# Performance work log

Measured on AMD Instinct MI355X. Metric: run time of the kernel, lower is better.

Reference implementation:

```python
import jax, jax.numpy as jnp
import numpy as np
import math

D_MODEL, D_K, D_V, N_HEADS = 1024, 64, 64, 16
B, LQ, LK = 4, 2048, 2048
LN_EPS = 1e-5


def setup_inputs() -> dict:
    key = jax.random.key(0)
    ks = jax.random.split(key, 8)
    s = 1.0 / math.sqrt(D_MODEL)
    return {
        "input_Q": jax.random.normal(ks[0], (B, LQ, D_MODEL), jnp.float32),
        "input_K": jax.random.normal(ks[1], (B, LK, D_MODEL), jnp.float32),
        "input_V": jax.random.normal(ks[2], (B, LK, D_MODEL), jnp.float32),
        "attn_mask": jax.random.randint(ks[3], (B, LQ, LK), 0, 2).astype(bool),
        # weights stored as [in, out] (torch Linear applies x @ W.T)
        "W_Q": jax.random.normal(ks[4], (D_MODEL, N_HEADS * D_K), jnp.float32) * s,
        "W_K": jax.random.normal(ks[5], (D_MODEL, N_HEADS * D_K), jnp.float32) * s,
        "W_V": jax.random.normal(ks[6], (D_MODEL, N_HEADS * D_V), jnp.float32) * s,
        "W_fc": jax.random.normal(ks[7], (N_HEADS * D_V, D_MODEL), jnp.float32) * s,
    }


def reference(input_Q, input_K, input_V, attn_mask, W_Q, W_K, W_V, W_fc):
    b, lq, _ = input_Q.shape
    lk = input_K.shape[1]
    # projections -> [b, len, h, d] -> [b, h, len, d]
    Q = (input_Q @ W_Q).reshape(b, lq, N_HEADS, D_K).transpose(0, 2, 1, 3)
    K = (input_K @ W_K).reshape(b, lk, N_HEADS, D_K).transpose(0, 2, 1, 3)
    V = (input_V @ W_V).reshape(b, lk, N_HEADS, D_V).transpose(0, 2, 1, 3)
    # scaled scores [b, h, q, k]
    scores = jnp.einsum("bhqd,bhkd->bhqk", Q, K) / math.sqrt(D_K)
    scores = jnp.where(attn_mask[:, None, :, :], -1e9, scores)
    attn = jax.nn.softmax(scores, axis=-1)
    # context [b, h, q, dv] -> [b, q, h*dv]
    ctx = jnp.einsum("bhqk,bhkd->bhqd", attn, V)
    ctx = ctx.transpose(0, 2, 1, 3).reshape(b, lq, N_HEADS * D_V)
    result = ctx @ W_fc
    x = result + input_Q
    mu = jnp.mean(x, axis=-1, keepdims=True)
    var = jnp.var(x, axis=-1, keepdims=True)
    res = (x - mu) / jnp.sqrt(var + LN_EPS)
    return res, attn
```

## Files before the change

### kernel.cpp

```cpp
#include <hip/hip_runtime.h>
#include <hip/hip_bf16.h>
#include <stdint.h>

#define DEVI __device__ __forceinline__

typedef __attribute__((ext_vector_type(8))) short bf16x8;
typedef __attribute__((ext_vector_type(4))) float f32x4;

static DEVI unsigned short f2bf(float f) {
  unsigned int u = __builtin_bit_cast(unsigned int, f);
  u = (u + 0x7FFFu + ((u >> 16) & 1u)) >> 16;
  return (unsigned short)u;
}

static DEVI void async16(const void* g, void* l) {
  __builtin_amdgcn_global_load_lds((__attribute__((address_space(1))) void*)(g),
                                   (__attribute__((address_space(3))) void*)(l),
                                   16, 0, 0);
}

__global__ __launch_bounds__(256) void cvt_kernel(const float* __restrict__ in,
                                                  unsigned short* __restrict__ out, int n4) {
  int i = blockIdx.x * 256 + threadIdx.x;
  if (i >= n4) return;
  float4 v = ((const float4*)in)[i];
  uint2 o;
  o.x = (unsigned)f2bf(v.x) | ((unsigned)f2bf(v.y) << 16);
  o.y = (unsigned)f2bf(v.z) | ((unsigned)f2bf(v.w) << 16);
  ((uint2*)out)[i] = o;
}

__global__ __launch_bounds__(256) void maskbits_kernel(const int* __restrict__ mask,
                                                       unsigned long long* __restrict__ mb) {
  size_t tg = (size_t)blockIdx.x * 256 + threadIdx.x;
  int v = mask[tg];
  unsigned long long bal = __ballot(v != 0);
  if ((threadIdx.x & 63) == 0) mb[tg >> 6] = bal;
}

__global__ __launch_bounds__(256) void wtrans_kernel(const float* __restrict__ W,
                                                     unsigned short* __restrict__ Wt) {
  __shared__ float t[32][33];
  const int bx = blockIdx.x * 32;
  const int by = blockIdx.y * 32;
  const int tx = threadIdx.x, ty = threadIdx.y;
#pragma unroll
  for (int i = 0; i < 32; i += 8) t[ty + i][tx] = W[(size_t)(by + ty + i) * 1024 + bx + tx];
  __syncthreads();
#pragma unroll
  for (int i = 0; i < 32; i += 8)
    Wt[(size_t)(bx + ty + i) * 1024 + by + tx] = f2bf(t[tx][ty + i]);
}

template <bool OUT_F32>
__global__ __launch_bounds__(256) void gemm_nt(const unsigned short* __restrict__ A, int lda,
                                               const unsigned short* __restrict__ B, int ldb,
                                               void* __restrict__ Cp, int ldc, int K) {
  __shared__ unsigned short As[128 * 64];
  __shared__ unsigned short Bs[128 * 64];
  const int tid = threadIdx.x;
  const int wave = tid >> 6, lane = tid & 63;
  const int m0 = blockIdx.x * 128, n0 = blockIdx.y * 128;
  const int wr = (wave >> 1) * 64, wc = (wave & 1) * 64;
  const int fr = lane & 15, fg = lane >> 4;
  f32x4 acc[4][4] = {};
  for (int kt = 0; kt < K; kt += 64) {
    __syncthreads();
#pragma unroll
    for (int it = 0; it < 4; ++it) {
      int id = it * 256 + tid;
      int row = id >> 3, ch = id & 7;
      async16(A + (size_t)(m0 + row) * lda + kt + ch * 8,
              (char*)As + (it * 256 + wave * 64) * 16);
      async16(B + (size_t)(n0 + row) * ldb + kt + ch * 8,
              (char*)Bs + (it * 256 + wave * 64) * 16);
    }
    __syncthreads();
#pragma unroll
    for (int ks = 0; ks < 2; ++ks) {
      bf16x8 af[4], bfr[4];
#pragma unroll
      for (int i = 0; i < 4; ++i)
        af[i] = *(const bf16x8*)(As + (wr + i * 16 + fr) * 64 + ks * 32 + fg * 8);
#pragma unroll
      for (int j = 0; j < 4; ++j)
        bfr[j] = *(const bf16x8*)(Bs + (wc + j * 16 + fr) * 64 + ks * 32 + fg * 8);
#pragma unroll
      for (int i = 0; i < 4; ++i)
#pragma unroll
        for (int j = 0; j < 4; ++j)
          acc[i][j] = __builtin_amdgcn_mfma_f32_16x16x32_bf16(af[i], bfr[j], acc[i][j], 0, 0, 0);
    }
  }
#pragma unroll
  for (int i = 0; i < 4; ++i)
#pragma unroll
    for (int j = 0; j < 4; ++j)
#pragma unroll
      for (int r = 0; r < 4; ++r) {
        int row = m0 + wr + i * 16 + fg * 4 + r;
        int col = n0 + wc + j * 16 + fr;
        if (OUT_F32)
          ((float*)Cp)[(size_t)row * ldc + col] = acc[i][j][r];
        else
          ((unsigned short*)Cp)[(size_t)row * ldc + col] = f2bf(acc[i][j][r]);
      }
}

__global__ __launch_bounds__(256) void vtrans_kernel(const unsigned short* __restrict__ Vp,
                                                     unsigned short* __restrict__ Vt) {
  __shared__ unsigned short t[64][72];
  const int bh = blockIdx.y;
  const int b = bh >> 4, h = bh & 15;
  const int l0 = blockIdx.x * 64;
  const int tid = threadIdx.x;
#pragma unroll
  for (int it = 0; it < 2; ++it) {
    int id = it * 256 + tid;
    int l = id >> 3, ch = id & 7;
    uint4 v = *(const uint4*)(Vp + (size_t)(b * 2048 + l0 + l) * 1024 + h * 64 + ch * 8);
    *(uint4*)(&t[l][ch * 8]) = v;
  }
  __syncthreads();
#pragma unroll
  for (int it = 0; it < 2; ++it) {
    int id = it * 256 + tid;
    int d = id >> 3, lc = id & 7;
    unsigned short o[8];
#pragma unroll
    for (int k = 0; k < 8; ++k) o[k] = t[lc * 8 + k][d];
    uint4 ov;
    ov.x = o[0] | ((unsigned)o[1] << 16);
    ov.y = o[2] | ((unsigned)o[3] << 16);
    ov.z = o[4] | ((unsigned)o[5] << 16);
    ov.w = o[6] | ((unsigned)o[7] << 16);
    *(uint4*)(Vt + ((size_t)bh * 64 + d) * 2048 + l0 + lc * 8) = ov;
  }
}

__global__ __launch_bounds__(256) void attn_kernel(
    const unsigned short* __restrict__ Qp, const unsigned short* __restrict__ Kp,
    const unsigned short* __restrict__ Vt, const unsigned long long* __restrict__ mb,
    float* __restrict__ attn_out, unsigned short* __restrict__ ctx) {
  __shared__ unsigned short Ks[2][4096];
  __shared__ unsigned short Vs[2][4096];
  __shared__ unsigned short Ps[4][1024];
  const int tid = threadIdx.x, wave = tid >> 6, lane = tid & 63;
  const int g = blockIdx.x;
  const int idx = g >> 3;
  const int bh = (g & 7) * 8 + (idx >> 5);
  const int b = bh >> 4, h = bh & 15;
  const int q0 = (idx & 31) * 64;
  const int fr = lane & 15, fg = lane >> 4;
  const int q = q0 + wave * 16 + fr;

  const int r0 = tid >> 3;
  const int chs = ((tid & 7) ^ (r0 & 7)) << 3;
  const unsigned short* kg = Kp + (size_t)(b * 2048 + r0) * 1024 + h * 64 + chs;
  const unsigned short* vg = Vt + (size_t)bh * 131072 + (size_t)r0 * 2048 + chs;

#define STAGE_K(buf, t)                                                    \
  do {                                                                     \
    const unsigned short* _k = kg + (size_t)(t) * 65536;                   \
    async16(_k, (char*)Ks[buf] + wave * 1024);                             \
    async16(_k + 32768, (char*)Ks[buf] + 4096 + wave * 1024);              \
  } while (0)
#define STAGE_V(buf, t)                                                    \
  do {                                                                     \
    const unsigned short* _v = vg + (t) * 64;                              \
    async16(_v, (char*)Vs[buf] + wave * 1024);                             \
    async16(_v + 65536, (char*)Vs[buf] + 4096 + wave * 1024);              \
  } while (0)

  const int c0 = (fg ^ (fr & 7)) << 3;
  const int c1 = ((4 + fg) ^ (fr & 7)) << 3;
  const int psw = (fr & 7) << 3;

  const unsigned short* qbase = Qp + (size_t)(b * 2048 + q) * 1024 + h * 64 + fg * 8;
  bf16x8 qa0 = *(const bf16x8*)(qbase);
  bf16x8 qa1 = *(const bf16x8*)(qbase + 32);

  const unsigned long long* mrow = mb + (size_t)(b * 2048 + q) * 32;
  const int msh = fg * 4;

  STAGE_K(0, 0);
  int cur = 0;
  float rsum = 0.f;
  for (int kt = 0; kt < 32; ++kt) {
    unsigned long long mw = mrow[kt];
    STAGE_K(cur ^ 1, (kt + 1) & 31);
    asm volatile("s_waitcnt vmcnt(3)" ::: "memory");
    __builtin_amdgcn_s_barrier();
    f32x4 s[4] = {};
#pragma unroll
    for (int j = 0; j < 4; ++j) {
      bf16x8 k0 = *(const bf16x8*)(&Ks[cur][(j * 16 + fr) * 64 + c0]);
      bf16x8 k1 = *(const bf16x8*)(&Ks[cur][(j * 16 + fr) * 64 + c1]);
      s[j] = __builtin_amdgcn_mfma_f32_16x16x32_bf16(k0, qa0, s[j], 0, 0, 0);
      s[j] = __builtin_amdgcn_mfma_f32_16x16x32_bf16(k1, qa1, s[j], 0, 0, 0);
    }
    unsigned mlo = (unsigned)mw, mhi = (unsigned)(mw >> 32);
#pragma unroll
    for (int j = 0; j < 4; ++j) {
      unsigned mj = ((j & 2) ? mhi : mlo) >> ((j & 1) * 16 + msh);
      rsum += ((mj & 1) ? 0.f : exp2f(s[j][0] * 0.18033688f));
      rsum += ((mj & 2) ? 0.f : exp2f(s[j][1] * 0.18033688f));
      rsum += ((mj & 4) ? 0.f : exp2f(s[j][2] * 0.18033688f));
      rsum += ((mj & 8) ? 0.f : exp2f(s[j][3] * 0.18033688f));
    }
    asm volatile("s_waitcnt lgkmcnt(0)" ::: "memory");
    __builtin_amdgcn_s_barrier();
    cur ^= 1;
  }
  rsum += __shfl_xor(rsum, 16);
  rsum += __shfl_xor(rsum, 32);
  const float rs = 1.0f / rsum;

  STAGE_V(cur, 0);
  asm volatile("s_waitcnt vmcnt(0)" ::: "memory");
  __builtin_amdgcn_s_barrier();
  f32x4 o[4] = {};
  unsigned short* pw = Ps[wave];
  float* aout = attn_out + ((size_t)(bh * 2048 + q)) * 2048 + fg * 4;

  for (int kt = 0; kt < 32; ++kt) {
    unsigned long long mw = mrow[kt];
    STAGE_K(cur ^ 1, (kt + 1) & 31);
    STAGE_V(cur ^ 1, (kt + 1) & 31);
    asm volatile("s_waitcnt vmcnt(21)" ::: "memory");
    __builtin_amdgcn_s_barrier();
    f32x4 s[4] = {};
#pragma unroll
    for (int j = 0; j < 4; ++j) {
      bf16x8 k0 = *(const bf16x8*)(&Ks[cur][(j * 16 + fr) * 64 + c0]);
      bf16x8 k1 = *(const bf16x8*)(&Ks[cur][(j * 16 + fr) * 64 + c1]);
      s[j] = __builtin_amdgcn_mfma_f32_16x16x32_bf16(k0, qa0, s[j], 0, 0, 0);
      s[j] = __builtin_amdgcn_mfma_f32_16x16x32_bf16(k1, qa1, s[j], 0, 0, 0);
    }
    unsigned mlo = (unsigned)mw, mhi = (unsigned)(mw >> 32);
#pragma unroll
    for (int j = 0; j < 4; ++j) {
      unsigned mj = ((j & 2) ? mhi : mlo) >> ((j & 1) * 16 + msh);
      float e0 = (mj & 1) ? 0.f : exp2f(s[j][0] * 0.18033688f) * rs;
      float e1 = (mj & 2) ? 0.f : exp2f(s[j][1] * 0.18033688f) * rs;
      float e2 = (mj & 4) ? 0.f : exp2f(s[j][2] * 0.18033688f) * rs;
      float e3 = (mj & 8) ? 0.f : exp2f(s[j][3] * 0.18033688f) * rs;
      f32x4 ev;
      ev[0] = e0; ev[1] = e1; ev[2] = e2; ev[3] = e3;
      __builtin_nontemporal_store(ev, (f32x4*)(aout + kt * 64 + j * 16));
      uint2 pv;
      pv.x = (unsigned)f2bf(e0) | ((unsigned)f2bf(e1) << 16);
      pv.y = (unsigned)f2bf(e2) | ((unsigned)f2bf(e3) << 16);
      *(uint2*)(pw + fr * 64 + ((j * 16 + fg * 4) ^ psw)) = pv;
    }
    asm volatile("s_waitcnt lgkmcnt(0)" ::: "memory");
    __builtin_amdgcn_sched_barrier(0);
    bf16x8 pa0 = *(const bf16x8*)(pw + fr * 64 + ((fg * 8) ^ psw));
    bf16x8 pa1 = *(const bf16x8*)(pw + fr * 64 + ((32 + fg * 8) ^ psw));
#pragma unroll
    for (int ct = 0; ct < 4; ++ct) {
      bf16x8 v0 = *(const bf16x8*)(&Vs[cur][(ct * 16 + fr) * 64 + c0]);
      bf16x8 v1 = *(const bf16x8*)(&Vs[cur][(ct * 16 + fr) * 64 + c1]);
      o[ct] = __builtin_amdgcn_mfma_f32_16x16x32_bf16(pa0, v0, o[ct], 0, 0, 0);
      o[ct] = __builtin_amdgcn_mfma_f32_16x16x32_bf16(pa1, v1, o[ct], 0, 0, 0);
    }
    asm volatile("s_waitcnt lgkmcnt(0)" ::: "memory");
    __builtin_amdgcn_s_barrier();
    cur ^= 1;
  }
#pragma unroll
  for (int ct = 0; ct < 4; ++ct)
#pragma unroll
    for (int r = 0; r < 4; ++r)
      ctx[(size_t)(b * 2048 + q0 + wave * 16 + fg * 4 + r) * 1024 + h * 64 + ct * 16 + fr] =
          f2bf(o[ct][r]);
#undef STAGE_K
#undef STAGE_V
}

__global__ __launch_bounds__(256) void ln_kernel(const float* __restrict__ resl,
                                                 const float* __restrict__ inQ,
                                                 float* __restrict__ out) {
  __shared__ float red[8];
  const int row = blockIdx.x, tid = threadIdx.x;
  const int wave = tid >> 6, lane = tid & 63;
  float4 xv = ((const float4*)(resl + (size_t)row * 1024))[tid];
  float4 qv = ((const float4*)(inQ + (size_t)row * 1024))[tid];
  float v0 = xv.x + qv.x, v1 = xv.y + qv.y, v2 = xv.z + qv.z, v3 = xv.w + qv.w;
  float s = v0 + v1 + v2 + v3;
  float s2 = v0 * v0 + v1 * v1 + v2 * v2 + v3 * v3;
#pragma unroll
  for (int off = 1; off < 64; off <<= 1) {
    s += __shfl_xor(s, off);
    s2 += __shfl_xor(s2, off);
  }
  if (lane == 0) { red[wave] = s; red[4 + wave] = s2; }
  __syncthreads();
  s = red[0] + red[1] + red[2] + red[3];
  s2 = red[4] + red[5] + red[6] + red[7];
  const float mu = s * (1.0f / 1024.0f);
  const float var = s2 * (1.0f / 1024.0f) - mu * mu;
  const float inv = rsqrtf(var + 1e-5f);
  float4 ov;
  ov.x = (v0 - mu) * inv;
  ov.y = (v1 - mu) * inv;
  ov.z = (v2 - mu) * inv;
  ov.w = (v3 - mu) * inv;
  ((float4*)(out + (size_t)row * 1024))[tid] = ov;
}

extern "C" void kernel_launch(void* const* d_in, const int* in_sizes, int n_in, void* d_out,
                              int out_size, void* d_ws, size_t ws_size, hipStream_t stream) {
  const float* inQ = (const float*)d_in[0];
  const float* inK = (const float*)d_in[1];
  const float* inV = (const float*)d_in[2];
  const int* mask = (const int*)d_in[3];
  const float* WQ = (const float*)d_in[4];
  const float* WK = (const float*)d_in[5];
  const float* WV = (const float*)d_in[6];
  const float* WF = (const float*)d_in[7];
  float* res = (float*)d_out;
  float* attn = res + (size_t)8192 * 1024;

  char* w = (char*)d_ws;
  unsigned short* inQb = (unsigned short*)w; w += (size_t)16777216;
  unsigned short* inKb = (unsigned short*)w; w += (size_t)16777216;
  unsigned short* inVb = (unsigned short*)w; w += (size_t)16777216;
  unsigned short* WQt = (unsigned short*)w; w += (size_t)2097152;
  unsigned short* WKt = (unsigned short*)w; w += (size_t)2097152;
  unsigned short* WVt = (unsigned short*)w; w += (size_t)2097152;
  unsigned short* WFt = (unsigned short*)w; w += (size_t)2097152;
  unsigned short* Qp  = (unsigned short*)w; w += (size_t)16777216;
  unsigned short* Kp  = (unsigned short*)w; w += (size_t)16777216;
  unsigned short* Vp  = (unsigned short*)w; w += (size_t)16777216;
  unsigned short* Vtb = (unsigned short*)w; w += (size_t)16777216;
  unsigned short* ctx = (unsigned short*)w; w += (size_t)16777216;
  float* resl = (float*)w; w += (size_t)33554432;
  unsigned long long* mbits = (unsigned long long*)inQb;

  cvt_kernel<<<8192, 256, 0, stream>>>(inQ, inQb, 2097152);
  cvt_kernel<<<8192, 256, 0, stream>>>(inK, inKb, 2097152);
  cvt_kernel<<<8192, 256, 0, stream>>>(inV, inVb, 2097152);
  dim3 wb(32, 8);
  wtrans_kernel<<<dim3(32, 32), wb, 0, stream>>>(WQ, WQt);
  wtrans_kernel<<<dim3(32, 32), wb, 0, stream>>>(WK, WKt);
  wtrans_kernel<<<dim3(32, 32), wb, 0, stream>>>(WV, WVt);
  wtrans_kernel<<<dim3(32, 32), wb, 0, stream>>>(WF, WFt);
  gemm_nt<false><<<dim3(64, 8), 256, 0, stream>>>(inQb, 1024, WQt, 1024, Qp, 1024, 1024);
  gemm_nt<false><<<dim3(64, 8), 256, 0, stream>>>(inKb, 1024, WKt, 1024, Kp, 1024, 1024);
  gemm_nt<false><<<dim3(64, 8), 256, 0, stream>>>(inVb, 1024, WVt, 1024, Vp, 1024, 1024);
  maskbits_kernel<<<65536, 256, 0, stream>>>(mask, mbits);
  vtrans_kernel<<<dim3(32, 64), 256, 0, stream>>>(Vp, Vtb);
  attn_kernel<<<2048, 256, 0, stream>>>(Qp, Kp, Vtb, mbits, attn, ctx);
  gemm_nt<true><<<dim3(64, 8), 256, 0, stream>>>(ctx, 1024, WFt, 1024, resl, 1024, 1024);
  ln_kernel<<<8192, 256, 0, stream>>>(resl, inQ, res);
}
```

Baseline: 535.2 us.

## Process two query tiles per wave in attention to halve K/V staging

Each wave now handles 32 query rows (two 16-row groups) instead of 16, so each workgroup covers 128 queries and the grid is halved, reusing each staged K/V tile across twice the queries. The softmax scale (log2e/sqrt(dk)) is folded into W_Q during weight transposition, which removes a multiply per score. Masked entries become exp2(-inf) rather than a select after exp. The bf16 packing now uses a v_cvt_pk_bf16_f32 instruction. Register pressure rises with doubled accumulators, though launch bounds hint at 4 blocks per SIMD.

Result: slower. 588.4 us (+9.9%).

```diff
diff --git a/kernel.cpp b/kernel.cpp
--- a/kernel.cpp
+++ b/kernel.cpp
@@ -39,7 +39,8 @@
 }
 
 __global__ __launch_bounds__(256) void wtrans_kernel(const float* __restrict__ W,
-                                                     unsigned short* __restrict__ Wt) {
+                                                     unsigned short* __restrict__ Wt,
+                                                     float scale) {
   __shared__ float t[32][33];
   const int bx = blockIdx.x * 32;
   const int by = blockIdx.y * 32;
@@ -49,7 +50,7 @@
   __syncthreads();
 #pragma unroll
   for (int i = 0; i < 32; i += 8)
-    Wt[(size_t)(bx + ty + i) * 1024 + by + tx] = f2bf(t[tx][ty + i]);
+    Wt[(size_t)(bx + ty + i) * 1024 + by + tx] = f2bf(t[tx][ty + i] * scale);
 }
 
 template <bool OUT_F32>
@@ -138,7 +139,7 @@
   }
 }
 
-__global__ __launch_bounds__(256) void attn_kernel(
+__global__ __launch_bounds__(256, 4) void attn_kernel(
     const unsigned short* __restrict__ Qp, const unsigned short* __restrict__ Kp,
     const unsigned short* __restrict__ Vt, const unsigned long long* __restrict__ mb,
     float* __restrict__ attn_out, unsigned short* __restrict__ ctx) {
@@ -148,11 +149,12 @@
   const int tid = threadIdx.x, wave = tid >> 6, lane = tid & 63;
   const int g = blockIdx.x;
   const int idx = g >> 3;
-  const int bh = (g & 7) * 8 + (idx >> 5);
+  const int bh = (g & 7) * 8 + (idx >> 4);
   const int b = bh >> 4, h = bh & 15;
-  const int q0 = (idx & 31) * 64;
+  const int q0 = (idx & 15) * 128;
   const int fr = lane & 15, fg = lane >> 4;
-  const int q = q0 + wave * 16 + fr;
+  const int qA = q0 + wave * 32 + fr;
+  const int qB = qA + 16;
 
   const int r0 = tid >> 3;
   const int chs = ((tid & 7) ^ (r0 & 7)) << 3;
@@ -176,94 +178,111 @@
   const int c1 = ((4 + fg) ^ (fr & 7)) << 3;
   const int psw = (fr & 7) << 3;
 
-  const unsigned short* qbase = Qp + (size_t)(b * 2048 + q) * 1024 + h * 64 + fg * 8;
-  bf16x8 qa0 = *(const bf16x8*)(qbase);
-  bf16x8 qa1 = *(const bf16x8*)(qbase + 32);
-
-  const unsigned long long* mrow = mb + (size_t)(b * 2048 + q) * 32;
+  const unsigned short* qbA = Qp + (size_t)(b * 2048 + qA) * 1024 + h * 64 + fg * 8;
+  const unsigned short* qbB = Qp + (size_t)(b * 2048 + qB) * 1024 + h * 64 + fg * 8;
+  bf16x8 qaA0 = *(const bf16x8*)(qbA);
+  bf16x8 qaA1 = *(const bf16x8*)(qbA + 32);
+  bf16x8 qaB0 = *(const bf16x8*)(qbB);
+  bf16x8 qaB1 = *(const bf16x8*)(qbB + 32);
+
+  const unsigned long long* mrowA = mb + (size_t)(b * 2048 + qA) * 32;
+  const unsigned long long* mrowB = mb + (size_t)(b * 2048 + qB) * 32;
   const int msh = fg * 4;
+  const float ninf = __uint_as_float(0xFF800000u);
+
+#define QK_BOTH(sA, sB)                                                         \
+  _Pragma("unroll") for (int j = 0; j < 4; ++j) {                               \
+    bf16x8 k0 = *(const bf16x8*)(&Ks[cur][(j * 16 + fr) * 64 + c0]);            \
+    bf16x8 k1 = *(const bf16x8*)(&Ks[cur][(j * 16 + fr) * 64 + c1]);            \
+    sA[j] = __builtin_amdgcn_mfma_f32_16x16x32_bf16(k0, qaA0, sA[j], 0, 0, 0);  \
+    sA[j] = __builtin_amdgcn_mfma_f32_16x16x32_bf16(k1, qaA1, sA[j], 0, 0, 0);  \
+    sB[j] = __builtin_amdgcn_mfma_f32_16x16x32_bf16(k0, qaB0, sB[j], 0, 0, 0);  \
+    sB[j] = __builtin_amdgcn_mfma_f32_16x16x32_bf16(k1, qaB1, sB[j], 0, 0, 0);  \
+  }
 
   STAGE_K(0, 0);
   int cur = 0;
-  float rsum = 0.f;
+  float rsumA = 0.f, rsumB = 0.f;
   for (int kt = 0; kt < 32; ++kt) {
-    unsigned long long mw = mrow[kt];
+    unsigned long long mwA = mrowA[kt], mwB = mrowB[kt];
     STAGE_K(cur ^ 1, (kt + 1) & 31);
-    asm volatile("s_waitcnt vmcnt(3)" ::: "memory");
+    asm volatile("s_waitcnt vmcnt(4)" ::: "memory");
     __builtin_amdgcn_s_barrier();
-    f32x4 s[4] = {};
-#pragma unroll
-    for (int j = 0; j < 4; ++j) {
-      bf16x8 k0 = *(const bf16x8*)(&Ks[cur][(j * 16 + fr) * 64 + c0]);
-      bf16x8 k1 = *(const bf16x8*)(&Ks[cur][(j * 16 + fr) * 64 + c1]);
-      s[j] = __builtin_amdgcn_mfma_f32_16x16x32_bf16(k0, qa0, s[j], 0, 0, 0);
-      s[j] = __builtin_amdgcn_mfma_f32_16x16x32_bf16(k1, qa1, s[j], 0, 0, 0);
-    }
-    unsigned mlo = (unsigned)mw, mhi = (unsigned)(mw >> 32);
-#pragma unroll
-    for (int j = 0; j < 4; ++j) {
-      unsigned mj = ((j & 2) ? mhi : mlo) >> ((j & 1) * 16 + msh);
-      rsum += ((mj & 1) ? 0.f : exp2f(s[j][0] * 0.18033688f));
-      rsum += ((mj & 2) ? 0.f : exp2f(s[j][1] * 0.18033688f));
-      rsum += ((mj & 4) ? 0.f : exp2f(s[j][2] * 0.18033688f));
-      rsum += ((mj & 8) ? 0.f : exp2f(s[j][3] * 0.18033688f));
+    f32x4 sA[4] = {}, sB[4] = {};
+    QK_BOTH(sA, sB)
+    {
+      unsigned lA = (unsigned)mwA, hA = (unsigned)(mwA >> 32);
+      unsigned lB = (unsigned)mwB, hB = (unsigned)(mwB >> 32);
+#pragma unroll
+      for (int j = 0; j < 4; ++j) {
+        unsigned mA = ((j & 2) ? hA : lA) >> ((j & 1) * 16 + msh);
+        unsigned mB = ((j & 2) ? hB : lB) >> ((j & 1) * 16 + msh);
+#pragma unroll
+        for (int r = 0; r < 4; ++r) {
+          rsumA += exp2f((mA & (1u << r)) ? ninf : sA[j][r]);
+          rsumB += exp2f((mB & (1u << r)) ? ninf : sB[j][r]);
+        }
+      }
     }
     asm volatile("s_waitcnt lgkmcnt(0)" ::: "memory");
     __builtin_amdgcn_s_barrier();
     cur ^= 1;
   }
-  rsum += __shfl_xor(rsum, 16);
-  rsum += __shfl_xor(rsum, 32);
-  const float rs = 1.0f / rsum;
+  rsumA += __shfl_xor(rsumA, 16);
+  rsumA += __shfl_xor(rsumA, 32);
+  rsumB += __shfl_xor(rsumB, 16);
+  rsumB += __shfl_xor(rsumB, 32);
+  const float rsA = 1.0f / rsumA;
+  const float rsB = 1.0f / rsumB;
 
   STAGE_V(cur, 0);
   asm volatile("s_waitcnt vmcnt(0)" ::: "memory");
   __builtin_amdgcn_s_barrier();
-  f32x4 o[4] = {};
+  f32x4 oA[4] = {}, oB[4] = {};
   unsigned short* pw = Ps[wave];
-  float* aout = attn_out + ((size_t)(bh * 2048 + q)) * 2048 + fg * 4;
+  float* aoutA = attn_out + ((size_t)(bh * 2048 + qA)) * 2048 + fg * 4;
+  float* aoutB = attn_out + ((size_t)(bh * 2048 + qB)) * 2048 + fg * 4;
+
+#define SM_PV(mw, sS, rsS, aoutS, oS)                                             \
+  {                                                                               \
+    unsigned mlo = (unsigned)mw, mhi = (unsigned)(mw >> 32);                      \
+    _Pragma("unroll") for (int j = 0; j < 4; ++j) {                               \
+      unsigned mj = ((j & 2) ? mhi : mlo) >> ((j & 1) * 16 + msh);                \
+      float e0 = exp2f((mj & 1u) ? ninf : sS[j][0]) * rsS;                        \
+      float e1 = exp2f((mj & 2u) ? ninf : sS[j][1]) * rsS;                        \
+      float e2 = exp2f((mj & 4u) ? ninf : sS[j][2]) * rsS;                        \
+      float e3 = exp2f((mj & 8u) ? ninf : sS[j][3]) * rsS;                        \
+      f32x4 ev;                                                                   \
+      ev[0] = e0; ev[1] = e1; ev[2] = e2; ev[3] = e3;                             \
+      __builtin_nontemporal_store(ev, (f32x4*)(aoutS + kt * 64 + j * 16));        \
+      unsigned pk0, pk1;                                                          \
+      asm("v_cvt_pk_bf16_f32 %0, %1, %2" : "=v"(pk0) : "v"(e0), "v"(e1));         \
+      asm("v_cvt_pk_bf16_f32 %0, %1, %2" : "=v"(pk1) : "v"(e2), "v"(e3));         \
+      uint2 pv; pv.x = pk0; pv.y = pk1;                                           \
+      *(uint2*)(pw + fr * 64 + ((j * 16 + fg * 4) ^ psw)) = pv;                   \
+    }                                                                             \
+    asm volatile("s_waitcnt lgkmcnt(0)" ::: "memory");                            \
+    __builtin_amdgcn_sched_barrier(0);                                            \
+    bf16x8 pa0 = *(const bf16x8*)(pw + fr * 64 + ((fg * 8) ^ psw));               \
+    bf16x8 pa1 = *(const bf16x8*)(pw + fr * 64 + ((32 + fg * 8) ^ psw));          \
+    _Pragma("unroll") for (int ct = 0; ct < 4; ++ct) {                            \
+      bf16x8 v0 = *(const bf16x8*)(&Vs[cur][(ct * 16 + fr) * 64 + c0]);           \
+      bf16x8 v1 = *(const bf16x8*)(&Vs[cur][(ct * 16 + fr) * 64 + c1]);           \
+      oS[ct] = __builtin_amdgcn_mfma_f32_16x16x32_bf16(pa0, v0, oS[ct], 0, 0, 0); \
+      oS[ct] = __builtin_amdgcn_mfma_f32_16x16x32_bf16(pa1, v1, oS[ct], 0, 0, 0); \
+    }                                                                             \
+  }
 
   for (int kt = 0; kt < 32; ++kt) {
-    unsigned long long mw = mrow[kt];
+    unsigned long long mwA = mrowA[kt], mwB = mrowB[kt];
     STAGE_K(cur ^ 1, (kt + 1) & 31);
     STAGE_V(cur ^ 1, (kt + 1) & 31);
-    asm volatile("s_waitcnt vmcnt(21)" ::: "memory");
+    asm volatile("s_waitcnt vmcnt(14)" ::: "memory");
     __builtin_amdgcn_s_barrier();
-    f32x4 s[4] = {};
-#pragma unroll
-    for (int j = 0; j < 4; ++j) {
-      bf16x8 k0 = *(const bf16x8*)(&Ks[cur][(j * 16 + fr) * 64 + c0]);
-      bf16x8 k1 = *(const bf16x8*)(&Ks[cur][(j * 16 + fr) * 64 + c1]);
-      s[j] = __builtin_amdgcn_mfma_f32_16x16x32_bf16(k0, qa0, s[j], 0, 0, 0);
-      s[j] = __builtin_amdgcn_mfma_f32_16x16x32_bf16(k1, qa1, s[j], 0, 0, 0);
-    }
-    unsigned mlo = (unsigned)mw, mhi = (unsigned)(mw >> 32);
-#pragma unroll
-    for (int j = 0; j < 4; ++j) {
-      unsigned mj = ((j & 2) ? mhi : mlo) >> ((j & 1) * 16 + msh);
-      float e0 = (mj & 1) ? 0.f : exp2f(s[j][0] * 0.18033688f) * rs;
-      float e1 = (mj & 2) ? 0.f : exp2f(s[j][1] * 0.18033688f) * rs;
-      float e2 = (mj & 4) ? 0.f : exp2f(s[j][2] * 0.18033688f) * rs;
-      float e3 = (mj & 8) ? 0.f : exp2f(s[j][3] * 0.18033688f) * rs;
-      f32x4 ev;
-      ev[0] = e0; ev[1] = e1; ev[2] = e2; ev[3] = e3;
-      __builtin_nontemporal_store(ev, (f32x4*)(aout + kt * 64 + j * 16));
-      uint2 pv;
-      pv.x = (unsigned)f2bf(e0) | ((unsigned)f2bf(e1) << 16);
-      pv.y = (unsigned)f2bf(e2) | ((unsigned)f2bf(e3) << 16);
-      *(uint2*)(pw + fr * 64 + ((j * 16 + fg * 4) ^ psw)) = pv;
-    }
-    asm volatile("s_waitcnt lgkmcnt(0)" ::: "memory");
-    __builtin_amdgcn_sched_barrier(0);
-    bf16x8 pa0 = *(const bf16x8*)(pw + fr * 64 + ((fg * 8) ^ psw));
-    bf16x8 pa1 = *(const bf16x8*)(pw + fr * 64 + ((32 + fg * 8) ^ psw));
-#pragma unroll
-    for (int ct = 0; ct < 4; ++ct) {
-      bf16x8 v0 = *(const bf16x8*)(&Vs[cur][(ct * 16 + fr) * 64 + c0]);
-      bf16x8 v1 = *(const bf16x8*)(&Vs[cur][(ct * 16 + fr) * 64 + c1]);
-      o[ct] = __builtin_amdgcn_mfma_f32_16x16x32_bf16(pa0, v0, o[ct], 0, 0, 0);
-      o[ct] = __builtin_amdgcn_mfma_f32_16x16x32_bf16(pa1, v1, o[ct], 0, 0, 0);
-    }
+    f32x4 sA[4] = {}, sB[4] = {};
+    QK_BOTH(sA, sB)
+    SM_PV(mwA, sA, rsA, aoutA, oA)
+    SM_PV(mwB, sB, rsB, aoutB, oB)
     asm volatile("s_waitcnt lgkmcnt(0)" ::: "memory");
     __builtin_amdgcn_s_barrier();
     cur ^= 1;
@@ -271,11 +290,16 @@
 #pragma unroll
   for (int ct = 0; ct < 4; ++ct)
 #pragma unroll
-    for (int r = 0; r < 4; ++r)
-      ctx[(size_t)(b * 2048 + q0 + wave * 16 + fg * 4 + r) * 1024 + h * 64 + ct * 16 + fr] =
-          f2bf(o[ct][r]);
+    for (int r = 0; r < 4; ++r) {
+      ctx[(size_t)(b * 2048 + qA - fr + fg * 4 + r) * 1024 + h * 64 + ct * 16 + fr] =
+          f2bf(oA[ct][r]);
+      ctx[(size_t)(b * 2048 + qB - fr + fg * 4 + r) * 1024 + h * 64 + ct * 16 + fr] =
+          f2bf(oB[ct][r]);
+    }
 #undef STAGE_K
 #undef STAGE_V
+#undef QK_BOTH
+#undef SM_PV
 }
 
 __global__ __launch_bounds__(256) void ln_kernel(const float* __restrict__ resl,
@@ -342,16 +366,16 @@
   cvt_kernel<<<8192, 256, 0, stream>>>(inK, inKb, 2097152);
   cvt_kernel<<<8192, 256, 0, stream>>>(inV, inVb, 2097152);
   dim3 wb(32, 8);
-  wtrans_kernel<<<dim3(32, 32), wb, 0, stream>>>(WQ, WQt);
-  wtrans_kernel<<<dim3(32, 32), wb, 0, stream>>>(WK, WKt);
-  wtrans_kernel<<<dim3(32, 32), wb, 0, stream>>>(WV, WVt);
-  wtrans_kernel<<<dim3(32, 32), wb, 0, stream>>>(WF, WFt);
+  wtrans_kernel<<<dim3(32, 32), wb, 0, stream>>>(WQ, WQt, 0.18033688f);
+  wtrans_kernel<<<dim3(32, 32), wb, 0, stream>>>(WK, WKt, 1.0f);
+  wtrans_kernel<<<dim3(32, 32), wb, 0, stream>>>(WV, WVt, 1.0f);
+  wtrans_kernel<<<dim3(32, 32), wb, 0, stream>>>(WF, WFt, 1.0f);
   gemm_nt<false><<<dim3(64, 8), 256, 0, stream>>>(inQb, 1024, WQt, 1024, Qp, 1024, 1024);
   gemm_nt<false><<<dim3(64, 8), 256, 0, stream>>>(inKb, 1024, WKt, 1024, Kp, 1024, 1024);
   gemm_nt<false><<<dim3(64, 8), 256, 0, stream>>>(inVb, 1024, WVt, 1024, Vp, 1024, 1024);
   maskbits_kernel<<<65536, 256, 0, stream>>>(mask, mbits);
   vtrans_kernel<<<dim3(32, 64), 256, 0, stream>>>(Vp, Vtb);
-  attn_kernel<<<2048, 256, 0, stream>>>(Qp, Kp, Vtb, mbits, attn, ctx);
+  attn_kernel<<<1024, 256, 0, stream>>>(Qp, Kp, Vtb, mbits, attn, ctx);
   gemm_nt<true><<<dim3(64, 8), 256, 0, stream>>>(ctx, 1024, WFt, 1024, resl, 1024, 1024);
   ln_kernel<<<8192, 256, 0, stream>>>(resl, inQ, res);
 }
```

## Widen attention blocks to 8 waves, fold softmax scale into W_Q, permlane P transpose

Applied to the files above, without the earlier changes.

The attention kernel now runs 512-thread blocks covering 128 queries, so each staged K/V tile is shared by 8 waves and each thread issues one async load per tile instead of two. The softmax scale (1/sqrt(dk)·log2e) is folded into the W_Q conversion, and masked positions become exp2(-inf), which removes a multiply and a select per element. The P matrix is converted with v_cvt_pk_bf16_f32 and rearranged through permlane swaps instead of a round trip through shared memory, dropping the Ps buffer and an LDS wait. The risks are the extra bf16 rounding of the pre-scaled Q, heavier register pressure from launch_bounds(512,4), and gfx950-specific instructions.

Measured after the change: 529.4 us. No clear change (-1.1%).

```diff
diff --git a/kernel.cpp b/kernel.cpp
--- a/kernel.cpp
+++ b/kernel.cpp
@@ -6,6 +6,7 @@
 
 typedef __attribute__((ext_vector_type(8))) short bf16x8;
 typedef __attribute__((ext_vector_type(4))) float f32x4;
+typedef __attribute__((ext_vector_type(4))) unsigned u32x4;
 
 static DEVI unsigned short f2bf(float f) {
   unsigned int u = __builtin_bit_cast(unsigned int, f);
@@ -39,7 +40,8 @@
 }
 
 __global__ __launch_bounds__(256) void wtrans_kernel(const float* __restrict__ W,
-                                                     unsigned short* __restrict__ Wt) {
+                                                     unsigned short* __restrict__ Wt,
+                                                     float scale) {
   __shared__ float t[32][33];
   const int bx = blockIdx.x * 32;
   const int by = blockIdx.y * 32;
@@ -49,7 +51,7 @@
   __syncthreads();
 #pragma unroll
   for (int i = 0; i < 32; i += 8)
-    Wt[(size_t)(bx + ty + i) * 1024 + by + tx] = f2bf(t[tx][ty + i]);
+    Wt[(size_t)(bx + ty + i) * 1024 + by + tx] = f2bf(t[tx][ty + i] * scale);
 }
 
 template <bool OUT_F32>
@@ -138,19 +140,18 @@
   }
 }
 
-__global__ __launch_bounds__(256) void attn_kernel(
+__global__ __launch_bounds__(512, 4) void attn_kernel(
     const unsigned short* __restrict__ Qp, const unsigned short* __restrict__ Kp,
     const unsigned short* __restrict__ Vt, const unsigned long long* __restrict__ mb,
     float* __restrict__ attn_out, unsigned short* __restrict__ ctx) {
   __shared__ unsigned short Ks[2][4096];
   __shared__ unsigned short Vs[2][4096];
-  __shared__ unsigned short Ps[4][1024];
   const int tid = threadIdx.x, wave = tid >> 6, lane = tid & 63;
   const int g = blockIdx.x;
   const int idx = g >> 3;
-  const int bh = (g & 7) * 8 + (idx >> 5);
+  const int bh = (g & 7) * 8 + (idx >> 4);
   const int b = bh >> 4, h = bh & 15;
-  const int q0 = (idx & 31) * 64;
+  const int q0 = (idx & 15) * 128;
   const int fr = lane & 15, fg = lane >> 4;
   const int q = q0 + wave * 16 + fr;
 
@@ -159,22 +160,11 @@
   const unsigned short* kg = Kp + (size_t)(b * 2048 + r0) * 1024 + h * 64 + chs;
   const unsigned short* vg = Vt + (size_t)bh * 131072 + (size_t)r0 * 2048 + chs;
 
-#define STAGE_K(buf, t)                                                    \
-  do {                                                                     \
-    const unsigned short* _k = kg + (size_t)(t) * 65536;                   \
-    async16(_k, (char*)Ks[buf] + wave * 1024);                             \
-    async16(_k + 32768, (char*)Ks[buf] + 4096 + wave * 1024);              \
-  } while (0)
-#define STAGE_V(buf, t)                                                    \
-  do {                                                                     \
-    const unsigned short* _v = vg + (t) * 64;                              \
-    async16(_v, (char*)Vs[buf] + wave * 1024);                             \
-    async16(_v + 65536, (char*)Vs[buf] + 4096 + wave * 1024);              \
-  } while (0)
+#define STAGE_K(buf, t) async16(kg + (size_t)(t) * 65536, (char*)Ks[buf] + wave * 1024)
+#define STAGE_V(buf, t) async16(vg + (t) * 64, (char*)Vs[buf] + wave * 1024)
 
   const int c0 = (fg ^ (fr & 7)) << 3;
   const int c1 = ((4 + fg) ^ (fr & 7)) << 3;
-  const int psw = (fr & 7) << 3;
 
   const unsigned short* qbase = Qp + (size_t)(b * 2048 + q) * 1024 + h * 64 + fg * 8;
   bf16x8 qa0 = *(const bf16x8*)(qbase);
@@ -182,6 +172,7 @@
 
   const unsigned long long* mrow = mb + (size_t)(b * 2048 + q) * 32;
   const int msh = fg * 4;
+  const float ninf = __uint_as_float(0xFF800000u);
 
   STAGE_K(0, 0);
   int cur = 0;
@@ -189,7 +180,7 @@
   for (int kt = 0; kt < 32; ++kt) {
     unsigned long long mw = mrow[kt];
     STAGE_K(cur ^ 1, (kt + 1) & 31);
-    asm volatile("s_waitcnt vmcnt(3)" ::: "memory");
+    asm volatile("s_waitcnt vmcnt(2)" ::: "memory");
     __builtin_amdgcn_s_barrier();
     f32x4 s[4] = {};
 #pragma unroll
@@ -203,10 +194,8 @@
 #pragma unroll
     for (int j = 0; j < 4; ++j) {
       unsigned mj = ((j & 2) ? mhi : mlo) >> ((j & 1) * 16 + msh);
-      rsum += ((mj & 1) ? 0.f : exp2f(s[j][0] * 0.18033688f));
-      rsum += ((mj & 2) ? 0.f : exp2f(s[j][1] * 0.18033688f));
-      rsum += ((mj & 4) ? 0.f : exp2f(s[j][2] * 0.18033688f));
-      rsum += ((mj & 8) ? 0.f : exp2f(s[j][3] * 0.18033688f));
+#pragma unroll
+      for (int r = 0; r < 4; ++r) rsum += exp2f((mj & (1u << r)) ? ninf : s[j][r]);
     }
     asm volatile("s_waitcnt lgkmcnt(0)" ::: "memory");
     __builtin_amdgcn_s_barrier();
@@ -220,14 +209,13 @@
   asm volatile("s_waitcnt vmcnt(0)" ::: "memory");
   __builtin_amdgcn_s_barrier();
   f32x4 o[4] = {};
-  unsigned short* pw = Ps[wave];
   float* aout = attn_out + ((size_t)(bh * 2048 + q)) * 2048 + fg * 4;
 
   for (int kt = 0; kt < 32; ++kt) {
     unsigned long long mw = mrow[kt];
     STAGE_K(cur ^ 1, (kt + 1) & 31);
     STAGE_V(cur ^ 1, (kt + 1) & 31);
-    asm volatile("s_waitcnt vmcnt(21)" ::: "memory");
+    asm volatile("s_waitcnt vmcnt(7)" ::: "memory");
     __builtin_amdgcn_s_barrier();
     f32x4 s[4] = {};
 #pragma unroll
@@ -238,25 +226,35 @@
       s[j] = __builtin_amdgcn_mfma_f32_16x16x32_bf16(k1, qa1, s[j], 0, 0, 0);
     }
     unsigned mlo = (unsigned)mw, mhi = (unsigned)(mw >> 32);
+    unsigned pk[4][2];
 #pragma unroll
     for (int j = 0; j < 4; ++j) {
       unsigned mj = ((j & 2) ? mhi : mlo) >> ((j & 1) * 16 + msh);
-      float e0 = (mj & 1) ? 0.f : exp2f(s[j][0] * 0.18033688f) * rs;
-      float e1 = (mj & 2) ? 0.f : exp2f(s[j][1] * 0.18033688f) * rs;
-      float e2 = (mj & 4) ? 0.f : exp2f(s[j][2] * 0.18033688f) * rs;
-      float e3 = (mj & 8) ? 0.f : exp2f(s[j][3] * 0.18033688f) * rs;
+      float e0 = exp2f((mj & 1u) ? ninf : s[j][0]) * rs;
+      float e1 = exp2f((mj & 2u) ? ninf : s[j][1]) * rs;
+      float e2 = exp2f((mj & 4u) ? ninf : s[j][2]) * rs;
+      float e3 = exp2f((mj & 8u) ? ninf : s[j][3]) * rs;
       f32x4 ev;
       ev[0] = e0; ev[1] = e1; ev[2] = e2; ev[3] = e3;
       __builtin_nontemporal_store(ev, (f32x4*)(aout + kt * 64 + j * 16));
-      uint2 pv;
-      pv.x = (unsigned)f2bf(e0) | ((unsigned)f2bf(e1) << 16);
-      pv.y = (unsigned)f2bf(e2) | ((unsigned)f2bf(e3) << 16);
-      *(uint2*)(pw + fr * 64 + ((j * 16 + fg * 4) ^ psw)) = pv;
-    }
-    asm volatile("s_waitcnt lgkmcnt(0)" ::: "memory");
-    __builtin_amdgcn_sched_barrier(0);
-    bf16x8 pa0 = *(const bf16x8*)(pw + fr * 64 + ((fg * 8) ^ psw));
-    bf16x8 pa1 = *(const bf16x8*)(pw + fr * 64 + ((32 + fg * 8) ^ psw));
+      asm("v_cvt_pk_bf16_f32 %0, %1, %2" : "=v"(pk[j][0]) : "v"(e0), "v"(e1));
+      asm("v_cvt_pk_bf16_f32 %0, %1, %2" : "=v"(pk[j][1]) : "v"(e2), "v"(e3));
+    }
+    unsigned x0 = pk[0][0], y0 = pk[1][0], x1 = pk[0][1], y1 = pk[1][1];
+    unsigned x2 = pk[2][0], y2 = pk[3][0], x3 = pk[2][1], y3 = pk[3][1];
+    asm("v_permlane32_swap_b32 %0, %1" : "+v"(x0), "+v"(y0));
+    asm("v_permlane16_swap_b32 %0, %1" : "+v"(x0), "+v"(y0));
+    asm("v_permlane32_swap_b32 %0, %1" : "+v"(x1), "+v"(y1));
+    asm("v_permlane16_swap_b32 %0, %1" : "+v"(x1), "+v"(y1));
+    asm("v_permlane32_swap_b32 %0, %1" : "+v"(x2), "+v"(y2));
+    asm("v_permlane16_swap_b32 %0, %1" : "+v"(x2), "+v"(y2));
+    asm("v_permlane32_swap_b32 %0, %1" : "+v"(x3), "+v"(y3));
+    asm("v_permlane16_swap_b32 %0, %1" : "+v"(x3), "+v"(y3));
+    u32x4 t0, t1;
+    t0[0] = x0; t0[1] = x1; t0[2] = y0; t0[3] = y1;
+    t1[0] = x2; t1[1] = x3; t1[2] = y2; t1[3] = y3;
+    bf16x8 pa0 = __builtin_bit_cast(bf16x8, t0);
+    bf16x8 pa1 = __builtin_bit_cast(bf16x8, t1);
 #pragma unroll
     for (int ct = 0; ct < 4; ++ct) {
       bf16x8 v0 = *(const bf16x8*)(&Vs[cur][(ct * 16 + fr) * 64 + c0]);
@@ -342,16 +340,16 @@
   cvt_kernel<<<8192, 256, 0, stream>>>(inK, inKb, 2097152);
   cvt_kernel<<<8192, 256, 0, stream>>>(inV, inVb, 2097152);
   dim3 wb(32, 8);
-  wtrans_kernel<<<dim3(32, 32), wb, 0, stream>>>(WQ, WQt);
-  wtrans_kernel<<<dim3(32, 32), wb, 0, stream>>>(WK, WKt);
-  wtrans_kernel<<<dim3(32, 32), wb, 0, stream>>>(WV, WVt);
-  wtrans_kernel<<<dim3(32, 32), wb, 0, stream>>>(WF, WFt);
+  wtrans_kernel<<<dim3(32, 32), wb, 0, stream>>>(WQ, WQt, 0.18033688f);
+  wtrans_kernel<<<dim3(32, 32), wb, 0, stream>>>(WK, WKt, 1.0f);
+  wtrans_kernel<<<dim3(32, 32), wb, 0, stream>>>(WV, WVt, 1.0f);
+  wtrans_kernel<<<dim3(32, 32), wb, 0, stream>>>(WF, WFt, 1.0f);
   gemm_nt<false><<<dim3(64, 8), 256, 0, stream>>>(inQb, 1024, WQt, 1024, Qp, 1024, 1024);
   gemm_nt<false><<<dim3(64, 8), 256, 0, stream>>>(inKb, 1024, WKt, 1024, Kp, 1024, 1024);
   gemm_nt<false><<<dim3(64, 8), 256, 0, stream>>>(inVb, 1024, WVt, 1024, Vp, 1024, 1024);
   maskbits_kernel<<<65536, 256, 0, stream>>>(mask, mbits);
   vtrans_kernel<<<dim3(32, 64), 256, 0, stream>>>(Vp, Vtb);
-  attn_kernel<<<2048, 256, 0, stream>>>(Qp, Kp, Vtb, mbits, attn, ctx);
+  attn_kernel<<<1024, 512, 0, stream>>>(Qp, Kp, Vtb, mbits, attn, ctx);
   gemm_nt<true><<<dim3(64, 8), 256, 0, stream>>>(ctx, 1024, WFt, 1024, resl, 1024, 1024);
   ln_kernel<<<8192, 256, 0, stream>>>(resl, inQ, res);
 }
```
